# Optimization experiments

Hardware: AMD Instinct MI355X
Metric: run time of the kernel (lower is better)

The kernel has to match this reference:

```python
import jax, jax.numpy as jnp
import numpy as np

EMBED = 1536
HEADS = 12
EPS = 1e-5


def _layernorm(x, gamma, beta):
    mu = x.mean(axis=-1, keepdims=True)
    var = ((x - mu) ** 2).mean(axis=-1, keepdims=True)
    return (x - mu) * jax.lax.rsqrt(var + EPS) * gamma + beta


def setup_inputs() -> dict:
    key = jax.random.key(0)
    ks = jax.random.split(key, 8)
    N, L, E = 8, 2048, EMBED
    x = jax.random.normal(ks[0], (N, L, E), dtype=jnp.float32)
    s = 0.02
    Wv = jax.random.normal(ks[1], (E, E), dtype=jnp.float32) * s
    Wk = jax.random.normal(ks[2], (E, E), dtype=jnp.float32) * s
    Wq = jax.random.normal(ks[3], (E, E), dtype=jnp.float32) * s
    Wo = jax.random.normal(ks[4], (E, E), dtype=jnp.float32) * s
    bo = jnp.zeros((E,), dtype=jnp.float32)
    gamma = jnp.ones((E,), dtype=jnp.float32)
    beta = jnp.zeros((E,), dtype=jnp.float32)
    return {"combined_embeddings": x, "Wv": Wv, "Wk": Wk, "Wq": Wq,
            "Wo": Wo, "bo": bo, "gamma": gamma, "beta": beta}


def reference(combined_embeddings, Wv, Wk, Wq, Wo, bo, gamma, beta):
    x = combined_embeddings
    N, L, E = x.shape
    H, hd = HEADS, E // HEADS
    # projections (torch Linear: x @ W^T), reshape to (N, H, L, hd)
    v = (x @ Wv.T).reshape(N, L, H, hd).transpose(0, 2, 1, 3)
    k = (x @ Wk.T).reshape(N, L, H, hd).transpose(0, 2, 1, 3)
    q = (x @ Wq.T).reshape(N, L, H, hd).transpose(0, 2, 1, 3)
    # NOTE: faithful to the source, einsum labels treat axis1 (heads) as q/k
    # and axis2 (sequence) as h -> heads-over-heads attention per position.
    energy = jnp.einsum('nqhd,nkhd->nhqk', q, k)  # (N, L, H, H)
    attention = jax.nn.softmax(energy / jnp.sqrt(jnp.float32(E)), axis=3)
    out = jnp.einsum('nhql,nlhd->nqhd', attention, v)  # (N, H, L, hd)
    out = out.transpose(0, 2, 1, 3).reshape(N, L, E)
    out = out @ Wo.T + bo
    out = _layernorm(out + x, gamma, beta)
    # small extra attention
    e_actions = out[:, 2:][None]          # (1, N, L-2, E)
    e_state = out.mean(axis=1)[None]      # (1, N, E)
    scores = jnp.matmul(e_state, jnp.swapaxes(e_actions, -2, -1))
    scores = scores / jnp.sqrt(jnp.float32(E))   # (1, N, N, L-2)
    weights = jax.nn.softmax(scores, axis=-1)
    attended = jnp.matmul(weights, e_actions)    # (1, N, N, E)
    return attended, weights
```

## Files before the change

### kernel.cpp

```cpp
#include <hip/hip_runtime.h>
#include <stdint.h>

typedef unsigned short u16;
typedef __bf16 bf16_t;
typedef bf16_t bf16x8 __attribute__((ext_vector_type(8)));
typedef float f32x4 __attribute__((ext_vector_type(4)));

#define E_DIM 1536
#define N_B 8
#define L_SEQ 2048
#define NT 2046
#define SCALE 0.025515518f
#define LN_EPS 1e-5f
#define NTILES 24
#define NXV 6291456
#define NWV 589824

__device__ __forceinline__ u16 f2b(float f) {
  union { float f; uint32_t u; } v; v.f = f;
  uint32_t u = v.u + 0x7FFFu + ((v.u >> 16) & 1u);
  return (u16)(u >> 16);
}
__device__ __forceinline__ float b2f(u16 h) {
  union { uint32_t u; float f; } v; v.u = ((uint32_t)h) << 16; return v.f;
}

__device__ __forceinline__ void gload16(const u16* g, const bf16_t* l) {
  __builtin_amdgcn_global_load_lds((const __attribute__((address_space(1))) void*)g,
                                   (__attribute__((address_space(3))) void*)l,
                                   16, 0, 0);
}

#define BAR()   __builtin_amdgcn_s_barrier()
#define SCHB()  __builtin_amdgcn_sched_barrier(0)
#define VM4()   asm volatile("s_waitcnt vmcnt(4)" ::: "memory")
#define VM0()   asm volatile("s_waitcnt vmcnt(0)" ::: "memory")

__global__ void cvt_all(const float* __restrict__ x,  const float* __restrict__ Wq,
                        const float* __restrict__ Wk, const float* __restrict__ Wv,
                        const float* __restrict__ Wo,
                        u16* __restrict__ xb,  u16* __restrict__ wqb,
                        u16* __restrict__ wkb, u16* __restrict__ wvb,
                        u16* __restrict__ wob)
{
  int i = blockIdx.x * 256 + threadIdx.x;
  const float* src; u16* dst; int o;
  if (i < NXV)              { src = x;  dst = xb;  o = i; }
  else if (i < NXV + NWV)   { src = Wq; dst = wqb; o = i - NXV; }
  else if (i < NXV + 2*NWV) { src = Wk; dst = wkb; o = i - NXV - NWV; }
  else if (i < NXV + 3*NWV) { src = Wv; dst = wvb; o = i - NXV - 2*NWV; }
  else                      { src = Wo; dst = wob; o = i - NXV - 3*NWV; }
  float4 f = ((const float4*)src)[o];
  ushort4 u;
  u.x = f2b(f.x); u.y = f2b(f.y); u.z = f2b(f.z); u.w = f2b(f.w);
  ((ushort4*)dst)[o] = u;
}

template<int FUSED>
__launch_bounds__(512, 2)
__global__ void gemm2c(const u16* __restrict__ Ag,
                       const u16* __restrict__ B0w, const u16* __restrict__ B1w,
                       const u16* __restrict__ B2w,
                       u16* __restrict__ C0, u16* __restrict__ C1, u16* __restrict__ C2,
                       const float* __restrict__ bias, const u16* __restrict__ resid16)
{
  extern __shared__ __attribute__((aligned(16))) bf16_t lds[];

  const int flat = (blockIdx.z * gridDim.y + blockIdx.y) * gridDim.x + blockIdx.x;
  const int xcd = flat & 7, bb_ = flat >> 3;
  const int gl = bb_ / 24, jj = bb_ % 24;
  const int g = gl * 8 + xcd;
  const int zz = g >> 4;
  const int gy = g & 15;
  const int tx = jj >> 2;
  const int ty = gy * 4 + (jj & 3);
  const int rowA = ty * 256, colB = tx * 256;

  const u16* Bg; u16* Cb;
  if (zz == 0)      { Bg = B0w; Cb = C0; }
  else if (zz == 1) { Bg = B1w; Cb = C1; }
  else              { Bg = B2w; Cb = C2; }

  const int tid = threadIdx.x;
  const int w = tid >> 6, lane = tid & 63;
  const int wr = w >> 2, wc = w & 3;

  const int rl = lane & 15, lsl = lane >> 4;
  const int sw8 = (lsl ^ ((rl >> 1) & 3)) * 8;
  const int arow = (wr * 128 + rl) * 32 + sw8;
  const int brow = (wc * 64 + rl) * 32 + sw8;

  const int r0s = tid >> 2, sps = tid & 3;
  const int sws = (sps ^ ((r0s >> 1) & 3)) * 8;
  const size_t sA0 = (size_t)(rowA + r0s) * E_DIM + sws;
  const size_t sA1 = (size_t)(rowA + 128 + r0s) * E_DIM + sws;
  const size_t sB0 = (size_t)(colB + r0s) * E_DIM + sws;
  const size_t sB1 = (size_t)(colB + 128 + r0s) * E_DIM + sws;
  const int wb0 = w * 512, wb1 = 4096 + w * 512;

  f32x4 acc[8][4];
#pragma unroll
  for (int m = 0; m < 8; ++m)
#pragma unroll
    for (int n = 0; n < 4; ++n)
#pragma unroll
      for (int q = 0; q < 4; ++q) acc[m][n][q] = 0.0f;

  gload16(Ag + sA0,      lds + 0     + wb0);  gload16(Ag + sA1,      lds + 0     + wb1);
  gload16(Bg + sB0,      lds + 32768 + wb0);  gload16(Bg + sB1,      lds + 32768 + wb1);
  gload16(Ag + sA0 + 32, lds + 8192  + wb0);  gload16(Ag + sA1 + 32, lds + 8192  + wb1);
  gload16(Bg + sB0 + 32, lds + 40960 + wb0);  gload16(Bg + sB1 + 32, lds + 40960 + wb1);
  gload16(Ag + sA0 + 64, lds + 16384 + wb0);  gload16(Ag + sA1 + 64, lds + 16384 + wb1);
  gload16(Bg + sB0 + 64, lds + 49152 + wb0);  gload16(Bg + sB1 + 64, lds + 49152 + wb1);
  VM4();
  BAR();

  bf16x8 a0[8], b0[4], a1[8], b1[4];
#pragma unroll
  for (int m = 0; m < 8; ++m) a0[m] = *(const bf16x8*)&lds[0 + arow + m * 512];
#pragma unroll
  for (int n = 0; n < 4; ++n) b0[n] = *(const bf16x8*)&lds[32768 + brow + n * 512];

  for (int t = 0; t < NTILES; ++t) {
    const int cur = t & 1, nxt = cur ^ 1;
    const int Ak1 = (cur * 2 + 1) * 8192, Bk1 = 32768 + (cur * 2 + 1) * 8192;
    const int AkN0 = nxt * 2 * 8192,      BkN0 = 32768 + nxt * 2 * 8192;
    const int AkN1 = (nxt * 2 + 1) * 8192, BkN1 = 32768 + (nxt * 2 + 1) * 8192;

#pragma unroll
    for (int m = 0; m < 8; ++m) a1[m] = *(const bf16x8*)&lds[Ak1 + arow + m * 512];
#pragma unroll
    for (int n = 0; n < 4; ++n) b1[n] = *(const bf16x8*)&lds[Bk1 + brow + n * 512];
    if (t + 1 < NTILES) {
      const size_t ko = (size_t)(t + 1) * 64 + 32;
      gload16(Ag + sA0 + ko, lds + AkN1 + wb0);  gload16(Ag + sA1 + ko, lds + AkN1 + wb1);
      gload16(Bg + sB0 + ko, lds + BkN1 + wb0);  gload16(Bg + sB1 + ko, lds + BkN1 + wb1);
    }
    SCHB();
    __builtin_amdgcn_s_setprio(1);
#pragma unroll
    for (int m = 0; m < 8; ++m)
#pragma unroll
      for (int n = 0; n < 4; ++n)
        acc[m][n] = __builtin_amdgcn_mfma_f32_16x16x32_bf16(a0[m], b0[n], acc[m][n], 0, 0, 0);
    __builtin_amdgcn_s_setprio(0);
    SCHB();
    if (t + 1 < NTILES) { VM4(); }
    BAR();

    if (t + 2 < NTILES) {
      const size_t ko = (size_t)(t + 2) * 64;
      gload16(Ag + sA0 + ko, lds + cur * 2 * 8192 + wb0);
      gload16(Ag + sA1 + ko, lds + cur * 2 * 8192 + wb1);
      gload16(Bg + sB0 + ko, lds + 32768 + cur * 2 * 8192 + wb0);
      gload16(Bg + sB1 + ko, lds + 32768 + cur * 2 * 8192 + wb1);
    }
    if (t + 1 < NTILES) {
#pragma unroll
      for (int m = 0; m < 8; ++m) a0[m] = *(const bf16x8*)&lds[AkN0 + arow + m * 512];
#pragma unroll
      for (int n = 0; n < 4; ++n) b0[n] = *(const bf16x8*)&lds[BkN0 + brow + n * 512];
    }
    SCHB();
    __builtin_amdgcn_s_setprio(1);
#pragma unroll
    for (int m = 0; m < 8; ++m)
#pragma unroll
      for (int n = 0; n < 4; ++n)
        acc[m][n] = __builtin_amdgcn_mfma_f32_16x16x32_bf16(a1[m], b1[n], acc[m][n], 0, 0, 0);
    __builtin_amdgcn_s_setprio(0);
    SCHB();
    if (t + 2 < NTILES)      { VM4(); }
    else if (t + 1 < NTILES) { VM0(); }
    BAR();
  }

  const int r0 = (lane >> 4) * 4;
#pragma unroll
  for (int m = 0; m < 8; ++m) {
#pragma unroll
    for (int n = 0; n < 4; ++n) {
      const int gcol = colB + wc * 64 + n * 16 + rl;
#pragma unroll
      for (int q = 0; q < 4; ++q) {
        const int grow = rowA + wr * 128 + m * 16 + r0 + q;
        const size_t idx = (size_t)grow * E_DIM + gcol;
        if (FUSED == 2)
          Cb[idx] = f2b(acc[m][n][q] + bias[gcol] + b2f(resid16[idx]));
        else
          Cb[idx] = f2b(acc[m][n][q]);
      }
    }
  }
}

__launch_bounds__(256)
__global__ void headmix(const u16* __restrict__ qb, const u16* __restrict__ kb,
                        const u16* __restrict__ vb, u16* __restrict__ aob)
{
  __shared__ float qs[12 * 132], ks2[12 * 132], vs[12 * 132];
  __shared__ float att[12][12];
  const int tid = threadIdx.x;
  const size_t base = (size_t)blockIdx.x * E_DIM;

  if (tid < 192) {
    const int i = tid >> 4, d0 = (tid & 15) * 8, p = i * 132 + d0;
    uint4 q4 = *(const uint4*)(qb + base + tid * 8);
    uint4 k4 = *(const uint4*)(kb + base + tid * 8);
    uint4 v4 = *(const uint4*)(vb + base + tid * 8);
#pragma unroll
    for (int c = 0; c < 4; ++c) {
      uint32_t qa = (&q4.x)[c], ka = (&k4.x)[c], va = (&v4.x)[c];
      qs[p + 2*c]     = b2f((u16)(qa & 0xFFFF));
      qs[p + 2*c + 1] = b2f((u16)(qa >> 16));
      ks2[p + 2*c]     = b2f((u16)(ka & 0xFFFF));
      ks2[p + 2*c + 1] = b2f((u16)(ka >> 16));
      vs[p + 2*c]     = b2f((u16)(va & 0xFFFF));
      vs[p + 2*c + 1] = b2f((u16)(va >> 16));
    }
  }
  __syncthreads();

  if (tid < 144) {
    int i = tid / 12, j = tid % 12;
    const float4* qr = (const float4*)&qs[i * 132];
    const float4* kr = (const float4*)&ks2[j * 132];
    float s = 0.f;
#pragma unroll 8
    for (int d4 = 0; d4 < 32; ++d4) {
      float4 a = qr[d4], b = kr[d4];
      s += a.x * b.x + a.y * b.y + a.z * b.z + a.w * b.w;
    }
    att[i][j] = s * SCALE;
  }
  __syncthreads();

  if (tid < 12) {
    float mx = att[tid][0];
#pragma unroll
    for (int j = 1; j < 12; ++j) mx = fmaxf(mx, att[tid][j]);
    float ev[12], sum = 0.f;
#pragma unroll
    for (int j = 0; j < 12; ++j) { ev[j] = expf(att[tid][j] - mx); sum += ev[j]; }
    float inv = 1.f / sum;
#pragma unroll
    for (int j = 0; j < 12; ++j) att[tid][j] = ev[j] * inv;
  }
  __syncthreads();

  if (tid < 192) {
    const int i = tid >> 4, d0 = (tid & 15) * 8;
    float o[8];
#pragma unroll
    for (int k = 0; k < 8; ++k) o[k] = 0.f;
#pragma unroll
    for (int j = 0; j < 12; ++j) {
      const float aij = att[i][j];
      const float4 v0 = *(const float4*)&vs[j * 132 + d0];
      const float4 v1 = *(const float4*)&vs[j * 132 + d0 + 4];
      o[0] += aij * v0.x; o[1] += aij * v0.y; o[2] += aij * v0.z; o[3] += aij * v0.w;
      o[4] += aij * v1.x; o[5] += aij * v1.y; o[6] += aij * v1.z; o[7] += aij * v1.w;
    }
    uint4 u;
#pragma unroll
    for (int c = 0; c < 4; ++c)
      (&u.x)[c] = (uint32_t)f2b(o[2*c]) | ((uint32_t)f2b(o[2*c+1]) << 16);
    *(uint4*)(aob + base + tid * 8) = u;
  }
}

__launch_bounds__(256)
__global__ void ln_kernel(const u16* __restrict__ p, u16* __restrict__ ho,
                          const float* __restrict__ gamma, const float* __restrict__ beta)
{
  __shared__ float rs[4], rq[4];
  __shared__ float mean_s, rstd_s;
  const int tid = threadIdx.x, w = tid >> 6, lane = tid & 63;
  const uint32_t* row = (const uint32_t*)(p + (size_t)blockIdx.x * E_DIM);
  uint32_t* orow = (uint32_t*)(ho + (size_t)blockIdx.x * E_DIM);

  float v[6], s = 0.f, sq = 0.f;
#pragma unroll
  for (int i = 0; i < 3; ++i) {
    uint32_t u = row[tid + i * 256];
    float lo = b2f((u16)(u & 0xFFFF)), hi = b2f((u16)(u >> 16));
    v[2*i] = lo; v[2*i+1] = hi;
    s += lo + hi; sq += lo * lo + hi * hi;
  }
#pragma unroll
  for (int off = 32; off > 0; off >>= 1) {
    s  += __shfl_down(s, off);
    sq += __shfl_down(sq, off);
  }
  if (lane == 0) { rs[w] = s; rq[w] = sq; }
  __syncthreads();
  if (tid == 0) {
    float S = rs[0] + rs[1] + rs[2] + rs[3];
    float Q = rq[0] + rq[1] + rq[2] + rq[3];
    float mu = S * (1.f / 1536.f);
    float var = Q * (1.f / 1536.f) - mu * mu;
    mean_s = mu; rstd_s = rsqrtf(var + LN_EPS);
  }
  __syncthreads();
  const float mu = mean_s, rstd = rstd_s;
#pragma unroll
  for (int i = 0; i < 3; ++i) {
    int j = tid + i * 256;
    float o0 = (v[2*i]   - mu) * rstd * gamma[2*j]   + beta[2*j];
    float o1 = (v[2*i+1] - mu) * rstd * gamma[2*j+1] + beta[2*j+1];
    orow[j] = (uint32_t)f2b(o0) | ((uint32_t)f2b(o1) << 16);
  }
}

__launch_bounds__(256)
__global__ void estate_partial(const u16* __restrict__ outp, float* __restrict__ part)
{
  const int tid = threadIdx.x;
  const int b = blockIdx.x, rc = blockIdx.y;
  if (tid >= 192) return;
  const uint4* base = (const uint4*)(outp + ((size_t)b * L_SEQ + rc * 64) * E_DIM);
  float a[8];
#pragma unroll
  for (int k = 0; k < 8; ++k) a[k] = 0.f;
  for (int r = 0; r < 64; ++r) {
    uint4 v = base[(size_t)r * 192 + tid];
#pragma unroll
    for (int c = 0; c < 4; ++c) {
      uint32_t u = (&v.x)[c];
      a[2*c]   += b2f((u16)(u & 0xFFFF));
      a[2*c+1] += b2f((u16)(u >> 16));
    }
  }
  float* dst = part + ((size_t)rc * N_B + b) * E_DIM + tid * 8;
#pragma unroll
  for (int k = 0; k < 8; ++k) dst[k] = a[k];
}
__global__ void estate_reduce(const float* __restrict__ part, float* __restrict__ est)
{
  const int i = blockIdx.x * 256 + threadIdx.x;
  if (i < N_B * E_DIM) {
    float s = 0.f;
#pragma unroll
    for (int z = 0; z < 32; ++z) s += part[(size_t)z * N_B * E_DIM + i];
    est[i] = s * (1.f / 2048.f);
  }
}

__launch_bounds__(256)
__global__ void scores_kernel(const u16* __restrict__ outp, const float* __restrict__ est,
                              float* __restrict__ wout)
{
  __shared__ float es[N_B * E_DIM];
  const int tid = threadIdx.x, wv = tid >> 6, lane = tid & 63;
  const int b = blockIdx.y;
  for (int i = tid; i < N_B * E_DIM; i += 256) es[i] = est[i];
  __syncthreads();

  for (int ti = 0; ti < 16; ++ti) {
    int t = blockIdx.x * 64 + wv * 16 + ti;
    if (t >= NT) continue;
    const uint32_t* row =
        (const uint32_t*)(outp + ((size_t)b * L_SEQ + 2 + t) * E_DIM);
    float a[8];
#pragma unroll
    for (int s = 0; s < 8; ++s) a[s] = 0.f;
    for (int c = 0; c < 12; ++c) {
      uint32_t pv = row[c * 64 + lane];
      float v0 = b2f((u16)(pv & 0xFFFF)), v1 = b2f((u16)(pv >> 16));
      int idx = (c * 64 + lane) * 2;
#pragma unroll
      for (int s = 0; s < 8; ++s)
        a[s] += es[s * E_DIM + idx] * v0 + es[s * E_DIM + idx + 1] * v1;
    }
#pragma unroll
    for (int off = 32; off > 0; off >>= 1)
#pragma unroll
      for (int s = 0; s < 8; ++s) a[s] += __shfl_down(a[s], off);
    if (lane == 0) {
#pragma unroll
      for (int s = 0; s < 8; ++s)
        wout[(size_t)(b * N_B + s) * NT + t] = a[s] * SCALE;
    }
  }
}

__launch_bounds__(256)
__global__ void softmax_w(float* __restrict__ wbase)
{
  float* p = wbase + (size_t)blockIdx.x * NT;
  __shared__ float r1[4], r2[4];
  __shared__ float bmax, bsum;
  const int tid = threadIdx.x, wv = tid >> 6, lane = tid & 63;

  float vals[8], mx = -1e30f;
#pragma unroll
  for (int i = 0; i < 8; ++i) {
    int t = tid + i * 256;
    vals[i] = (t < NT) ? p[t] : -1e30f;
    mx = fmaxf(mx, vals[i]);
  }
#pragma unroll
  for (int off = 32; off > 0; off >>= 1) mx = fmaxf(mx, __shfl_down(mx, off));
  if (lane == 0) r1[wv] = mx;
  __syncthreads();
  if (tid == 0) bmax = fmaxf(fmaxf(r1[0], r1[1]), fmaxf(r1[2], r1[3]));
  __syncthreads();
  mx = bmax;

  float sum = 0.f;
#pragma unroll
  for (int i = 0; i < 8; ++i) {
    int t = tid + i * 256;
    if (t < NT) { vals[i] = expf(vals[i] - mx); sum += vals[i]; }
  }
#pragma unroll
  for (int off = 32; off > 0; off >>= 1) sum += __shfl_down(sum, off);
  if (lane == 0) r2[wv] = sum;
  __syncthreads();
  if (tid == 0) bsum = r2[0] + r2[1] + r2[2] + r2[3];
  __syncthreads();
  const float inv = 1.f / bsum;
#pragma unroll
  for (int i = 0; i < 8; ++i) {
    int t = tid + i * 256;
    if (t < NT) p[t] = vals[i] * inv;
  }
}

__launch_bounds__(256)
__global__ void attended_partial(const u16* __restrict__ outp, const float* __restrict__ wts,
                                 float* __restrict__ part)
{
  __shared__ float wl[8][64];
  const int tid = threadIdx.x;
  const int b = blockIdx.x, tc = blockIdx.y;
  const int t0 = tc * 64;
  const int cnt = (NT - t0 < 64) ? (NT - t0) : 64;

  for (int i = tid; i < 8 * 64; i += 256) {
    int s = i >> 6, tt = i & 63;
    wl[s][tt] = (tt < cnt) ? wts[(size_t)(b * N_B + s) * NT + t0 + tt] : 0.f;
  }
  __syncthreads();
  if (tid >= 192) return;

  const uint4* base = (const uint4*)(outp + ((size_t)b * L_SEQ + 2 + t0) * E_DIM);
  float a[8][8];
#pragma unroll
  for (int s = 0; s < 8; ++s)
#pragma unroll
    for (int k = 0; k < 8; ++k) a[s][k] = 0.f;

  for (int tt = 0; tt < cnt; ++tt) {
    uint4 v = base[(size_t)tt * 192 + tid];
    float e[8];
#pragma unroll
    for (int c = 0; c < 4; ++c) {
      uint32_t u = (&v.x)[c];
      e[2*c]   = b2f((u16)(u & 0xFFFF));
      e[2*c+1] = b2f((u16)(u >> 16));
    }
#pragma unroll
    for (int s = 0; s < 8; ++s) {
      const float wv = wl[s][tt];
#pragma unroll
      for (int k = 0; k < 8; ++k) a[s][k] += wv * e[k];
    }
  }
#pragma unroll
  for (int s = 0; s < 8; ++s) {
    float* dst = part + (((size_t)tc * N_B + b) * N_B + s) * E_DIM + tid * 8;
#pragma unroll
    for (int k = 0; k < 8; ++k) dst[k] = a[s][k];
  }
}
__global__ void attended_reduce(const float* __restrict__ part, float* __restrict__ outp)
{
  const int i = blockIdx.x * 256 + threadIdx.x;
  float s = 0.f;
#pragma unroll
  for (int z = 0; z < 32; ++z) s += part[(size_t)z * N_B * N_B * E_DIM + i];
  outp[i] = s;
}

extern "C" void kernel_launch(void* const* d_in, const int* in_sizes, int n_in,
                              void* d_out, int out_size, void* d_ws, size_t ws_size,
                              hipStream_t stream)
{
  (void)in_sizes; (void)n_in; (void)out_size; (void)ws_size;
  const float* x     = (const float*)d_in[0];
  const float* Wv    = (const float*)d_in[1];
  const float* Wk    = (const float*)d_in[2];
  const float* Wq    = (const float*)d_in[3];
  const float* Wo    = (const float*)d_in[4];
  const float* bo    = (const float*)d_in[5];
  const float* gamma = (const float*)d_in[6];
  const float* beta  = (const float*)d_in[7];
  float* out = (float*)d_out;

  char* ws = (char*)d_ws;
  size_t off = 0;
  auto alloc = [&](size_t bytes) -> void* {
    void* p = ws + off;
    off += (bytes + 255) & ~(size_t)255;
    return p;
  };
  const size_t ME = (size_t)16384 * E_DIM;
  const size_t WE = (size_t)E_DIM * E_DIM;
  u16*   xb     = (u16*)alloc(ME * 2);
  u16*   wqb    = (u16*)alloc(WE * 2);
  u16*   wkb    = (u16*)alloc(WE * 2);
  u16*   wvb    = (u16*)alloc(WE * 2);
  u16*   wob    = (u16*)alloc(WE * 2);
  u16*   qb     = (u16*)alloc(ME * 2);
  u16*   kb     = (u16*)alloc(ME * 2);
  u16*   vb     = (u16*)alloc(ME * 2);
  u16*   aob    = (u16*)alloc(ME * 2);
  u16*   lnbufh = (u16*)alloc(ME * 2);
  float* est    = (float*)alloc((size_t)N_B * E_DIM * 4);
  float* estp   = (float*)alloc((size_t)32 * N_B * E_DIM * 4);
  float* attp   = (float*)alloc((size_t)32 * N_B * N_B * E_DIM * 4);

  float* wout = out + 98304;

  hipFuncSetAttribute(reinterpret_cast<const void*>(gemm2c<0>),
                      hipFuncAttributeMaxDynamicSharedMemorySize, 131072);
  hipFuncSetAttribute(reinterpret_cast<const void*>(gemm2c<2>),
                      hipFuncAttributeMaxDynamicSharedMemorySize, 131072);

  cvt_all<<<dim3((NXV + 4 * NWV) / 256), 256, 0, stream>>>(
      x, Wq, Wk, Wv, Wo, xb, wqb, wkb, wvb, wob);

  gemm2c<0><<<dim3(6, 64, 3), 512, 131072, stream>>>(
      xb, wqb, wkb, wvb, qb, kb, vb, nullptr, nullptr);

  headmix<<<dim3(16384), 256, 0, stream>>>(qb, kb, vb, aob);

  gemm2c<2><<<dim3(6, 64, 1), 512, 131072, stream>>>(
      aob, wob, wob, wob, lnbufh, lnbufh, lnbufh, bo, xb);

  u16* lnh = aob;
  ln_kernel<<<dim3(16384), 256, 0, stream>>>(lnbufh, lnh, gamma, beta);

  estate_partial<<<dim3(8, 32), 256, 0, stream>>>(lnh, estp);
  estate_reduce<<<dim3(48), 256, 0, stream>>>(estp, est);

  scores_kernel<<<dim3(32, 8), 256, 0, stream>>>(lnh, est, wout);
  softmax_w<<<dim3(64), 256, 0, stream>>>(wout);

  attended_partial<<<dim3(8, 32), 256, 0, stream>>>(lnh, wout, attp);
  attended_reduce<<<dim3(384), 256, 0, stream>>>(attp, out);
}
```

Before: 500.9 us.

## Restructure GEMM main loop into quadrant-wise MFMA phases with staggered prefetch

The bf16 GEMM main loop now runs in four phases per K-tile. Each phase loads one quadrant of A/B fragments (both K halves) from LDS and issues the MFMAs for that 128x32 sub-block of the warp tile. Global-to-LDS prefetches are spread across the phases, with lgkmcnt waits and barriers between them, and launch bounds drop from 2 to 1 blocks per CU. The goal is finer interleaving of LDS reads, global loads and MFMA work, and fewer live fragment registers. The cost is more barriers per iteration and possibly lower occupancy.

```diff
diff --git a/kernel.cpp b/kernel.cpp
--- a/kernel.cpp
+++ b/kernel.cpp
@@ -33,7 +33,9 @@
 
 #define BAR()   __builtin_amdgcn_s_barrier()
 #define SCHB()  __builtin_amdgcn_sched_barrier(0)
-#define VM4()   asm volatile("s_waitcnt vmcnt(4)" ::: "memory")
+#define LG0()   asm volatile("s_waitcnt lgkmcnt(0)" ::: "memory")
+#define LG8()   asm volatile("s_waitcnt lgkmcnt(8)" ::: "memory")
+#define VM6()   asm volatile("s_waitcnt vmcnt(6)" ::: "memory")
 #define VM0()   asm volatile("s_waitcnt vmcnt(0)" ::: "memory")
 
 __global__ void cvt_all(const float* __restrict__ x,  const float* __restrict__ Wq,
@@ -57,12 +59,12 @@
 }
 
 template<int FUSED>
-__launch_bounds__(512, 2)
-__global__ void gemm2c(const u16* __restrict__ Ag,
-                       const u16* __restrict__ B0w, const u16* __restrict__ B1w,
-                       const u16* __restrict__ B2w,
-                       u16* __restrict__ C0, u16* __restrict__ C1, u16* __restrict__ C2,
-                       const float* __restrict__ bias, const u16* __restrict__ resid16)
+__launch_bounds__(512, 1)
+__global__ void gemmq(const u16* __restrict__ Ag,
+                      const u16* __restrict__ B0w, const u16* __restrict__ B1w,
+                      const u16* __restrict__ B2w,
+                      u16* __restrict__ C0, u16* __restrict__ C1, u16* __restrict__ C2,
+                      const float* __restrict__ bias, const u16* __restrict__ resid16)
 {
   extern __shared__ __attribute__((aligned(16))) bf16_t lds[];
 
@@ -98,6 +100,19 @@
   const size_t sB1 = (size_t)(colB + 128 + r0s) * E_DIM + sws;
   const int wb0 = w * 512, wb1 = 4096 + w * 512;
 
+  auto stA = [&](int u, int kh) {
+    const size_t ko = (size_t)u * 64 + kh * 32;
+    bf16_t* d = lds + ((u & 1) * 2 + kh) * 8192;
+    gload16(Ag + sA0 + ko, d + wb0);
+    gload16(Ag + sA1 + ko, d + wb1);
+  };
+  auto stB = [&](int u, int kh) {
+    const size_t ko = (size_t)u * 64 + kh * 32;
+    bf16_t* d = lds + 32768 + ((u & 1) * 2 + kh) * 8192;
+    gload16(Bg + sB0 + ko, d + wb0);
+    gload16(Bg + sB1 + ko, d + wb1);
+  };
+
   f32x4 acc[8][4];
 #pragma unroll
   for (int m = 0; m < 8; ++m)
@@ -106,72 +121,65 @@
 #pragma unroll
       for (int q = 0; q < 4; ++q) acc[m][n][q] = 0.0f;
 
-  gload16(Ag + sA0,      lds + 0     + wb0);  gload16(Ag + sA1,      lds + 0     + wb1);
-  gload16(Bg + sB0,      lds + 32768 + wb0);  gload16(Bg + sB1,      lds + 32768 + wb1);
-  gload16(Ag + sA0 + 32, lds + 8192  + wb0);  gload16(Ag + sA1 + 32, lds + 8192  + wb1);
-  gload16(Bg + sB0 + 32, lds + 40960 + wb0);  gload16(Bg + sB1 + 32, lds + 40960 + wb1);
-  gload16(Ag + sA0 + 64, lds + 16384 + wb0);  gload16(Ag + sA1 + 64, lds + 16384 + wb1);
-  gload16(Bg + sB0 + 64, lds + 49152 + wb0);  gload16(Bg + sB1 + 64, lds + 49152 + wb1);
-  VM4();
+  bf16x8 aF0[8], aF1[8], bF0[4], bF1[4];
+
+  auto rdAf = [&](bf16x8 (&d)[8], int buf, int h) {
+#pragma unroll
+    for (int mp = 0; mp < 4; ++mp)
+#pragma unroll
+      for (int kk = 0; kk < 2; ++kk)
+        d[mp * 2 + kk] = *(const bf16x8*)&lds[(buf * 2 + kk) * 8192 + arow + (h * 4 + mp) * 512];
+  };
+  auto rdBf = [&](bf16x8 (&d)[4], int buf, int c) {
+#pragma unroll
+    for (int np = 0; np < 2; ++np)
+#pragma unroll
+      for (int kk = 0; kk < 2; ++kk)
+        d[np * 2 + kk] = *(const bf16x8*)&lds[32768 + (buf * 2 + kk) * 8192 + brow + (c * 2 + np) * 512];
+  };
+  auto mfq = [&](const bf16x8 (&af)[8], const bf16x8 (&bf)[4], int h, int c) {
+    __builtin_amdgcn_s_setprio(1);
+#pragma unroll
+    for (int kk = 0; kk < 2; ++kk)
+#pragma unroll
+      for (int mp = 0; mp < 4; ++mp)
+#pragma unroll
+        for (int np = 0; np < 2; ++np)
+          acc[h * 4 + mp][c * 2 + np] = __builtin_amdgcn_mfma_f32_16x16x32_bf16(
+              af[mp * 2 + kk], bf[np * 2 + kk], acc[h * 4 + mp][c * 2 + np], 0, 0, 0);
+    __builtin_amdgcn_s_setprio(0);
+  };
+
+  stA(0, 0); stB(0, 0); stA(0, 1); stB(0, 1);
+  stA(1, 0); stB(1, 0); stB(1, 1);
+  VM6();
   BAR();
 
-  bf16x8 a0[8], b0[4], a1[8], b1[4];
-#pragma unroll
-  for (int m = 0; m < 8; ++m) a0[m] = *(const bf16x8*)&lds[0 + arow + m * 512];
-#pragma unroll
-  for (int n = 0; n < 4; ++n) b0[n] = *(const bf16x8*)&lds[32768 + brow + n * 512];
-
   for (int t = 0; t < NTILES; ++t) {
-    const int cur = t & 1, nxt = cur ^ 1;
-    const int Ak1 = (cur * 2 + 1) * 8192, Bk1 = 32768 + (cur * 2 + 1) * 8192;
-    const int AkN0 = nxt * 2 * 8192,      BkN0 = 32768 + nxt * 2 * 8192;
-    const int AkN1 = (nxt * 2 + 1) * 8192, BkN1 = 32768 + (nxt * 2 + 1) * 8192;
-
-#pragma unroll
-    for (int m = 0; m < 8; ++m) a1[m] = *(const bf16x8*)&lds[Ak1 + arow + m * 512];
-#pragma unroll
-    for (int n = 0; n < 4; ++n) b1[n] = *(const bf16x8*)&lds[Bk1 + brow + n * 512];
-    if (t + 1 < NTILES) {
-      const size_t ko = (size_t)(t + 1) * 64 + 32;
-      gload16(Ag + sA0 + ko, lds + AkN1 + wb0);  gload16(Ag + sA1 + ko, lds + AkN1 + wb1);
-      gload16(Bg + sB0 + ko, lds + BkN1 + wb0);  gload16(Bg + sB1 + ko, lds + BkN1 + wb1);
-    }
-    SCHB();
-    __builtin_amdgcn_s_setprio(1);
-#pragma unroll
-    for (int m = 0; m < 8; ++m)
-#pragma unroll
-      for (int n = 0; n < 4; ++n)
-        acc[m][n] = __builtin_amdgcn_mfma_f32_16x16x32_bf16(a0[m], b0[n], acc[m][n], 0, 0, 0);
-    __builtin_amdgcn_s_setprio(0);
-    SCHB();
-    if (t + 1 < NTILES) { VM4(); }
+    const int cur = t & 1;
+
+    rdAf(aF0, cur, 0); rdBf(bF0, cur, 0);
+    if (t + 1 < NTILES) stA(t + 1, 1);
+    LG8(); BAR(); LG0(); SCHB();
+    mfq(aF0, bF0, 0, 0);
     BAR();
 
-    if (t + 2 < NTILES) {
-      const size_t ko = (size_t)(t + 2) * 64;
-      gload16(Ag + sA0 + ko, lds + cur * 2 * 8192 + wb0);
-      gload16(Ag + sA1 + ko, lds + cur * 2 * 8192 + wb1);
-      gload16(Bg + sB0 + ko, lds + 32768 + cur * 2 * 8192 + wb0);
-      gload16(Bg + sB1 + ko, lds + 32768 + cur * 2 * 8192 + wb1);
-    }
-    if (t + 1 < NTILES) {
-#pragma unroll
-      for (int m = 0; m < 8; ++m) a0[m] = *(const bf16x8*)&lds[AkN0 + arow + m * 512];
-#pragma unroll
-      for (int n = 0; n < 4; ++n) b0[n] = *(const bf16x8*)&lds[BkN0 + brow + n * 512];
-    }
-    SCHB();
-    __builtin_amdgcn_s_setprio(1);
-#pragma unroll
-    for (int m = 0; m < 8; ++m)
-#pragma unroll
-      for (int n = 0; n < 4; ++n)
-        acc[m][n] = __builtin_amdgcn_mfma_f32_16x16x32_bf16(a1[m], b1[n], acc[m][n], 0, 0, 0);
-    __builtin_amdgcn_s_setprio(0);
-    SCHB();
-    if (t + 2 < NTILES)      { VM4(); }
-    else if (t + 1 < NTILES) { VM0(); }
+    rdBf(bF1, cur, 1);
+    BAR(); LG0(); SCHB();
+    mfq(aF0, bF1, 0, 1);
+    BAR();
+
+    rdAf(aF1, cur, 1);
+    if (t + 2 < NTILES) stB(t + 2, 0);
+    BAR(); LG0(); SCHB();
+    mfq(aF1, bF1, 1, 1);
+    BAR();
+
+    if (t + 2 < NTILES) { stB(t + 2, 1); stA(t + 2, 0); }
+    BAR(); LG0(); SCHB();
+    mfq(aF1, bF0, 1, 0);
+    if (t < NTILES - 2)      { VM6(); }
+    else if (t == NTILES - 2) { VM0(); }
     BAR();
   }
 
@@ -523,20 +531,20 @@
 
   float* wout = out + 98304;
 
-  hipFuncSetAttribute(reinterpret_cast<const void*>(gemm2c<0>),
+  hipFuncSetAttribute(reinterpret_cast<const void*>(gemmq<0>),
                       hipFuncAttributeMaxDynamicSharedMemorySize, 131072);
-  hipFuncSetAttribute(reinterpret_cast<const void*>(gemm2c<2>),
+  hipFuncSetAttribute(reinterpret_cast<const void*>(gemmq<2>),
                       hipFuncAttributeMaxDynamicSharedMemorySize, 131072);
 
   cvt_all<<<dim3((NXV + 4 * NWV) / 256), 256, 0, stream>>>(
       x, Wq, Wk, Wv, Wo, xb, wqb, wkb, wvb, wob);
 
-  gemm2c<0><<<dim3(6, 64, 3), 512, 131072, stream>>>(
+  gemmq<0><<<dim3(6, 64, 3), 512, 131072, stream>>>(
       xb, wqb, wkb, wvb, qb, kb, vb, nullptr, nullptr);
 
   headmix<<<dim3(16384), 256, 0, stream>>>(qb, kb, vb, aob);
 
-  gemm2c<2><<<dim3(6, 64, 1), 512, 131072, stream>>>(
+  gemmq<2><<<dim3(6, 64, 1), 512, 131072, stream>>>(
       aob, wob, wob, wob, lnbufh, lnbufh, lnbufh, bo, xb);
 
   u16* lnh = aob;
```

After: 508.7 us. About the same (+1.5%).
